# Performance work log

Measured on AMD Instinct MI355X. Metric: run time of the kernel, lower is better.

Reference implementation:

```python
import jax, jax.numpy as jnp
import numpy as np

B, L, H = 16, 4096, 256

def setup_inputs() -> dict:
    key = jax.random.key(0)
    k1, k2, k3 = jax.random.split(key, 3)
    scale = 1.0 / np.sqrt(H)
    x = jax.random.normal(k1, (B, L, H), dtype=jnp.float32)
    Wv = jax.random.normal(k2, (H, H), dtype=jnp.float32) * scale  # value_proj weight (torch Linear: y = x @ W.T)
    Wo = jax.random.normal(k3, (H, H), dtype=jnp.float32) * scale  # out_proj weight
    return {"x": x, "Wv": Wv, "Wo": Wo}

def reference(x, Wv, Wo):
    # x: [B, L, H]
    Bx, Lx, Hx = x.shape
    # Causal uniform-average 'attention' matrix: T[i, j] = 1/(i+1) for j <= i, else 0.
    tril = jnp.tril(jnp.ones((Lx, Lx), dtype=x.dtype))
    counts = jnp.arange(1, Lx + 1, dtype=x.dtype)[:, None]  # row-wise counts = i+1
    T = tril / counts
    # v = out_proj(value_proj(x)); torch Linear applies W.T on the right
    v = (x @ Wv.T) @ Wo.T                       # [B, L, H]
    # mixed[b, i] = mean over j <= i of v[b, j]  (== causal cumulative mean)
    mixed = jnp.einsum('ij,bjh->bih', T, v)     # [B, L, H]
    # dropout is identity in eval mode; pre_ln residual
    return x + mixed
```

## Files before the change

kernel.cpp:

```cpp
#include <hip/hip_runtime.h>
#include <hip/hip_bf16.h>


#define B_  16
#define L_  4096
#define H_  256
#define M_  (B_*L_)
#define CH  64
#define CHROWS 64

typedef short short8 __attribute__((ext_vector_type(8)));
typedef float f32x4  __attribute__((ext_vector_type(4)));

__device__ __forceinline__ unsigned short f2bf(float f) {
  unsigned int u = __builtin_bit_cast(unsigned int, f);
  u += 0x7fffu + ((u >> 16) & 1u);
  return (unsigned short)(u >> 16);
}

__global__ void fuse_w_kernel(const float* __restrict__ Wv,
                              const float* __restrict__ Wo,
                              unsigned short* __restrict__ Wbf) {
  __shared__ float wo[H_];
  int h = blockIdx.x, t = threadIdx.x;
  wo[t] = Wo[h*H_ + t];
  __syncthreads();
  float acc = 0.f;
  #pragma unroll 8
  for (int m = 0; m < H_; ++m) acc += wo[m] * Wv[m*H_ + t];
  Wbf[h*H_ + t] = f2bf(acc);
}

__global__ void partial_kernel(const float* __restrict__ x, float* __restrict__ P) {
  int c = blockIdx.x, b = blockIdx.y, t = threadIdx.x;
  const float* p = x + ((size_t)(b*L_ + c*CHROWS))*H_ + t;
  float s = 0.f;
  #pragma unroll 8
  for (int r = 0; r < CHROWS; ++r) s += p[(size_t)r*H_];
  P[(b*CH + c)*H_ + t] = s;
}

__global__ void scan_kernel(const float* __restrict__ P, float* __restrict__ O) {
  int b = blockIdx.x, t = threadIdx.x;
  float run = 0.f;
  #pragma unroll
  for (int c = 0; c < CH; ++c) {
    int idx = (b*CH + c)*H_ + t;
    O[idx] = run;
    run += P[idx];
  }
}

#define BM 128

__global__ __launch_bounds__(512, 2) void gemm_fused(
    const float* __restrict__ x,
    const unsigned short* __restrict__ Wbf,
    const float* __restrict__ O,
    float* __restrict__ out) {
  __shared__ __align__(16) unsigned short As[BM * H_];
  char* Asb = (char*)As;

  const int tid = threadIdx.x;
  const int rowBase = blockIdx.x * BM;
  const int b  = rowBase >> 12;
  const int ri = rowBase & (L_ - 1);

  if (tid < H_) {
    const int t = tid;
    float run = O[((b << 6) + (ri >> 6)) * H_ + t];
    const float* xp = x + (size_t)rowBase * H_ + t;
    #pragma unroll 8
    for (int r = 0; r < BM; ++r) {
      run += xp[(size_t)r * H_];
      int pc = (2*t) ^ ((r & 7) << 4);
      *(unsigned short*)(Asb + r*512 + pc) = f2bf(run);
    }
  }
  __syncthreads();

  const int wave = tid >> 6, lane = tid & 63;
  const int wr = wave >> 2, wc = wave & 3;
  const int lrow = lane & 15;
  const int lk   = lane >> 4;

  f32x4 acc[4][4] = {};

  for (int k0 = 0; k0 < H_; k0 += 64) {
    #pragma unroll
    for (int ks = 0; ks < 2; ++ks) {
      short8 bf[4];
      #pragma unroll
      for (int n = 0; n < 4; ++n) {
        int wrow = wc*64 + n*16 + lrow;
        bf[n] = *(const short8*)(Wbf + (size_t)wrow*H_ + k0 + ks*32 + lk*8);
      }
      short8 af[4];
      #pragma unroll
      for (int i = 0; i < 4; ++i) {
        int ar = wr*64 + i*16 + lrow;
        int cb = (k0*2 + ks*64 + lk*16) ^ ((ar & 7) << 4);
        af[i] = *(const short8*)(Asb + ar*512 + cb);
      }
      #pragma unroll
      for (int i = 0; i < 4; ++i)
        #pragma unroll
        for (int n = 0; n < 4; ++n)
          acc[i][n] = __builtin_amdgcn_mfma_f32_16x16x32_bf16(af[i], bf[n], acc[i][n], 0, 0, 0);
    }
  }

  #pragma unroll
  for (int i = 0; i < 4; ++i) {
    #pragma unroll
    for (int j4 = 0; j4 < 4; ++j4) {
      int row = rowBase + wr*64 + i*16 + lk*4 + j4;
      float scale = 1.0f / (float)((row & (L_ - 1)) + 1);
      size_t rb = (size_t)row * H_;
      #pragma unroll
      for (int n = 0; n < 4; ++n) {
        int col = wc*64 + n*16 + lrow;
        out[rb + col] = x[rb + col] + acc[i][n][j4] * scale;
      }
    }
  }
}

extern "C" void kernel_launch(void* const* d_in, const int* in_sizes, int n_in,
                              void* d_out, int out_size, void* d_ws, size_t ws_size,
                              hipStream_t stream) {
  const float* x  = (const float*)d_in[0];
  const float* Wv = (const float*)d_in[1];
  const float* Wo = (const float*)d_in[2];
  float* out = (float*)d_out;

  char* ws = (char*)d_ws;
  unsigned short* Wbf = (unsigned short*)ws;
  float* P = (float*)(ws + (size_t)H_*H_*2);
  float* Off = P + B_*CH*H_;

  hipLaunchKernelGGL(fuse_w_kernel,  dim3(H_),     dim3(H_), 0, stream, Wv, Wo, Wbf);
  hipLaunchKernelGGL(partial_kernel, dim3(CH, B_), dim3(H_), 0, stream, x, P);
  hipLaunchKernelGGL(scan_kernel,    dim3(B_),     dim3(H_), 0, stream, P, Off);
  hipLaunchKernelGGL(gemm_fused,     dim3(M_/BM),  dim3(512), 0, stream,
                     x, Wbf, Off, out);
}
```

Before: 90.86 us.

## Move the causal prefix scan from GEMM inputs to MFMA accumulators

Result: faster. 84.92 us (-6.5%).

```diff
diff --git a/kernel.cpp b/kernel.cpp
--- a/kernel.cpp
+++ b/kernel.cpp
@@ -8,14 +8,20 @@
 #define M_  (B_*L_)
 #define CH  64
 #define CHROWS 64
+#define BM 128
 
-typedef short short8 __attribute__((ext_vector_type(8)));
-typedef float f32x4  __attribute__((ext_vector_type(4)));
+typedef short short4v __attribute__((ext_vector_type(4)));
+typedef short short8  __attribute__((ext_vector_type(8)));
+typedef float f32x4   __attribute__((ext_vector_type(4)));
 
 __device__ __forceinline__ unsigned short f2bf(float f) {
   unsigned int u = __builtin_bit_cast(unsigned int, f);
   u += 0x7fffu + ((u >> 16) & 1u);
   return (unsigned short)(u >> 16);
+}
+__device__ __forceinline__ float bf2f(unsigned short s) {
+  unsigned int u = ((unsigned int)s) << 16;
+  return __builtin_bit_cast(float, u);
 }
 
 __global__ void fuse_w_kernel(const float* __restrict__ Wv,
@@ -51,76 +57,112 @@
   }
 }
 
-#define BM 128
-
-__global__ __launch_bounds__(512, 2) void gemm_fused(
+__global__ __launch_bounds__(512, 4) void main_kernel(
     const float* __restrict__ x,
     const unsigned short* __restrict__ Wbf,
-    const float* __restrict__ O,
+    const float* __restrict__ Op,
     float* __restrict__ out) {
-  __shared__ __align__(16) unsigned short As[BM * H_];
-  char* Asb = (char*)As;
+  extern __shared__ char smem[];
+  float* zbuf = (float*)(smem + 65536);
+  float* csum = zbuf + 256;
 
   const int tid = threadIdx.x;
+  const int lane = tid & 63, wave = tid >> 6;
   const int rowBase = blockIdx.x * BM;
-  const int b  = rowBase >> 12;
-  const int ri = rowBase & (L_ - 1);
 
-  if (tid < H_) {
-    const int t = tid;
-    float run = O[((b << 6) + (ri >> 6)) * H_ + t];
-    const float* xp = x + (size_t)rowBase * H_ + t;
-    #pragma unroll 8
-    for (int r = 0; r < BM; ++r) {
-      run += xp[(size_t)r * H_];
-      int pc = (2*t) ^ ((r & 7) << 4);
-      *(unsigned short*)(Asb + r*512 + pc) = f2bf(run);
-    }
+  #pragma unroll 4
+  for (int it = 0; it < 16; ++it) {
+    int r = it*8 + wave;
+    const float4 v = *(const float4*)(x + (size_t)(rowBase + r)*H_ + lane*4);
+    short4v s;
+    s[0] = (short)f2bf(v.x); s[1] = (short)f2bf(v.y);
+    s[2] = (short)f2bf(v.z); s[3] = (short)f2bf(v.w);
+    *(short4v*)(smem + r*512 + ((lane*8) ^ ((r & 7) << 4))) = s;
   }
   __syncthreads();
 
-  const int wave = tid >> 6, lane = tid & 63;
+  if (tid < H_) {
+    const float* op = Op + (size_t)blockIdx.x * 2 * H_;
+    float z = 0.f;
+    #pragma unroll 4
+    for (int kk = 0; kk < 32; ++kk) {
+      short8 w8 = *(const short8*)(Wbf + (size_t)tid*H_ + kk*8);
+      #pragma unroll
+      for (int e = 0; e < 8; ++e)
+        z += op[kk*8 + e] * bf2f((unsigned short)w8[e]);
+    }
+    zbuf[tid] = z;
+  }
+
   const int wr = wave >> 2, wc = wave & 3;
-  const int lrow = lane & 15;
-  const int lk   = lane >> 4;
+  const int lrow = lane & 15, g = lane >> 4;
 
   f32x4 acc[4][4] = {};
-
+  #pragma unroll
   for (int k0 = 0; k0 < H_; k0 += 64) {
     #pragma unroll
     for (int ks = 0; ks < 2; ++ks) {
-      short8 bf[4];
+      short8 bfr[4], af[4];
       #pragma unroll
       for (int n = 0; n < 4; ++n) {
         int wrow = wc*64 + n*16 + lrow;
-        bf[n] = *(const short8*)(Wbf + (size_t)wrow*H_ + k0 + ks*32 + lk*8);
+        bfr[n] = *(const short8*)(Wbf + (size_t)wrow*H_ + k0 + ks*32 + g*8);
       }
-      short8 af[4];
       #pragma unroll
       for (int i = 0; i < 4; ++i) {
         int ar = wr*64 + i*16 + lrow;
-        int cb = (k0*2 + ks*64 + lk*16) ^ ((ar & 7) << 4);
-        af[i] = *(const short8*)(Asb + ar*512 + cb);
+        int cb = (k0*2 + ks*64 + g*16) ^ ((ar & 7) << 4);
+        af[i] = *(const short8*)(smem + ar*512 + cb);
       }
       #pragma unroll
       for (int i = 0; i < 4; ++i)
         #pragma unroll
         for (int n = 0; n < 4; ++n)
-          acc[i][n] = __builtin_amdgcn_mfma_f32_16x16x32_bf16(af[i], bf[n], acc[i][n], 0, 0, 0);
+          acc[i][n] = __builtin_amdgcn_mfma_f32_16x16x32_bf16(af[i], bfr[n], acc[i][n], 0, 0, 0);
     }
   }
 
   #pragma unroll
+  for (int n = 0; n < 4; ++n) {
+    float run = 0.f;
+    #pragma unroll
+    for (int i = 0; i < 4; ++i) {
+      f32x4 a = acc[i][n];
+      a[1] += a[0]; a[2] += a[1]; a[3] += a[2];
+      float Bv = a[3];
+      float v = Bv;
+      float t = __shfl_up(v, 16);
+      if (lane >= 16) v += t;
+      t = __shfl_up(v, 32);
+      if (lane >= 32) v += t;
+      float gex = v - Bv;
+      float tot = __shfl(v, lrow + 48);
+      float addv = gex + run;
+      a[0] += addv; a[1] += addv; a[2] += addv; a[3] += addv;
+      acc[i][n] = a;
+      run += tot;
+    }
+    if (wr == 0 && g == 0) csum[wc*64 + n*16 + lrow] = run;
+  }
+  __syncthreads();
+
+  float base[4];
+  #pragma unroll
+  for (int n = 0; n < 4; ++n) {
+    int c = wc*64 + n*16 + lrow;
+    base[n] = zbuf[c] + (wr ? csum[c] : 0.f);
+  }
+  #pragma unroll
   for (int i = 0; i < 4; ++i) {
     #pragma unroll
-    for (int j4 = 0; j4 < 4; ++j4) {
-      int row = rowBase + wr*64 + i*16 + lk*4 + j4;
-      float scale = 1.0f / (float)((row & (L_ - 1)) + 1);
+    for (int q = 0; q < 4; ++q) {
+      int row = rowBase + wr*64 + i*16 + g*4 + q;
+      float scale = 1.0f / (float)((row & (L_-1)) + 1);
       size_t rb = (size_t)row * H_;
       #pragma unroll
       for (int n = 0; n < 4; ++n) {
-        int col = wc*64 + n*16 + lrow;
-        out[rb + col] = x[rb + col] + acc[i][n][j4] * scale;
+        int c = wc*64 + n*16 + lrow;
+        out[rb + c] = x[rb + c] + (acc[i][n][q] + base[n]) * scale;
       }
     }
   }
@@ -136,12 +178,12 @@
 
   char* ws = (char*)d_ws;
   unsigned short* Wbf = (unsigned short*)ws;
-  float* P = (float*)(ws + (size_t)H_*H_*2);
-  float* Off = P + B_*CH*H_;
+  float* P  = (float*)(ws + 131072);
+  float* Op = (float*)(ws + 131072 + 1048576);
 
   hipLaunchKernelGGL(fuse_w_kernel,  dim3(H_),     dim3(H_), 0, stream, Wv, Wo, Wbf);
   hipLaunchKernelGGL(partial_kernel, dim3(CH, B_), dim3(H_), 0, stream, x, P);
-  hipLaunchKernelGGL(scan_kernel,    dim3(B_),     dim3(H_), 0, stream, P, Off);
-  hipLaunchKernelGGL(gemm_fused,     dim3(M_/BM),  dim3(512), 0, stream,
-                     x, Wbf, Off, out);
+  hipLaunchKernelGGL(scan_kernel,    dim3(B_),     dim3(H_), 0, stream, P, Op);
+  hipLaunchKernelGGL(main_kernel,    dim3(M_/BM),  dim3(512), 67584, stream,
+                     x, Wbf, Op, out);
 }
```
